# Performance work log

Measured on AMD Instinct MI355X. Metric: run time of the kernel, lower is better.

Reference implementation:

```python
import jax, jax.numpy as jnp
import numpy as np

HEADS = 16
HEAD_DIM = 64  # hidden_dim // heads = 1024 // 16


def setup_inputs() -> dict:
    key = jax.random.key(0)
    ks = jax.random.split(key, 7)
    B, S, D = 2, 2048, 1024
    x = jax.random.normal(ks[0], (B, S, D), dtype=jnp.float32)
    mask = jax.random.randint(ks[1], (B, 1, S, S), 0, 2, dtype=jnp.int32)
    scale = 1.0 / np.sqrt(D)
    Wq = jax.random.normal(ks[2], (D, D), dtype=jnp.float32) * scale
    Wk = jax.random.normal(ks[3], (D, D), dtype=jnp.float32) * scale
    Wv = jax.random.normal(ks[4], (D, D), dtype=jnp.float32) * scale
    Wo = jax.random.normal(ks[5], (D, D), dtype=jnp.float32) * scale
    bo = jnp.zeros((D,), dtype=jnp.float32)
    return {"x": x, "mask": mask, "Wq": Wq, "Wk": Wk, "Wv": Wv, "Wo": Wo, "bo": bo}


def _split_heads(t):
    # (B, S, D) -> (B, H, S, Hd)
    B, S, D = t.shape
    return t.reshape(B, S, HEADS, HEAD_DIM).transpose(0, 2, 1, 3)


def reference(x, mask, Wq, Wk, Wv, Wo, bo):
    B, S, D = x.shape
    # torch nn.Linear: y = x @ W.T (weights stored [out, in])
    q = _split_heads(x @ Wq.T)
    k = _split_heads(x @ Wk.T)
    v = _split_heads(x @ Wv.T)
    scores = jnp.einsum("bhqd,bhkd->bhqk", q, k) / jnp.sqrt(jnp.float32(HEAD_DIM))
    scores = jnp.where(mask == 1, jnp.float32(-1e9), scores)
    attn = jax.nn.softmax(scores, axis=-1)
    # dropout p=0.0 (eval) -> identity
    out = jnp.einsum("bhqk,bhkd->bhqd", attn, v)
    out = out.transpose(0, 2, 1, 3).reshape(B, S, D)
    return out @ Wo.T + bo
```

## Files before the change

kernel.cpp:

```cpp
#include <hip/hip_runtime.h>
#include <hip/hip_bf16.h>

typedef __attribute__((ext_vector_type(4))) float f32x4;
typedef __attribute__((ext_vector_type(16))) float f32x16;
typedef __attribute__((ext_vector_type(8))) short bf16x8;

#define MFMA16(a, b, c) __builtin_amdgcn_mfma_f32_16x16x32_bf16(a, b, c, 0, 0, 0)
#define MFMA32(a, b, c) __builtin_amdgcn_mfma_f32_32x32x16_bf16(a, b, c, 0, 0, 0)

#define AS1(p) ((const __attribute__((address_space(1))) void*)(p))
#define AS3(p) ((__attribute__((address_space(3))) void*)(p))

#define SWZK(r) ((((r) & 7)) ^ ((((r) >> 3) & 1) << 2))

__device__ __forceinline__ unsigned short f2bf(float f) {
  union { float f; unsigned u; } x; x.f = f;
  unsigned r = x.u + 0x7fffu + ((x.u >> 16) & 1u);
  return (unsigned short)(r >> 16);
}

__global__ __launch_bounds__(256) void convert_inputs(
    const float* __restrict__ x, const float* __restrict__ wq,
    const float* __restrict__ wk, const float* __restrict__ wv,
    const float* __restrict__ wo, const int* __restrict__ mask,
    unsigned short* __restrict__ dst, unsigned char* __restrict__ mdst) {
  const int NX = 4194304, NW = 1048576;
  if (blockIdx.x < 4096) {
    const int i = blockIdx.x * 256 + threadIdx.x;
    const long base = (long)i * 8;
    const float* src; long off; float sc = 1.0f;
    if (base < NX) { src = x; off = base; }
    else {
      long j = base - NX; int wsI = (int)(j >> 20); off = j & (NW - 1);
      src = (wsI == 0) ? wq : (wsI == 1) ? wk : (wsI == 2) ? wv : wo;
      if (wsI == 0) sc = 0.18033688f;
    }
    float4 a = *(const float4*)(src + off);
    float4 b = *(const float4*)(src + off + 4);
    uint4 o;
    o.x = (unsigned)f2bf(a.x * sc) | ((unsigned)f2bf(a.y * sc) << 16);
    o.y = (unsigned)f2bf(a.z * sc) | ((unsigned)f2bf(a.w * sc) << 16);
    o.z = (unsigned)f2bf(b.x * sc) | ((unsigned)f2bf(b.y * sc) << 16);
    o.w = (unsigned)f2bf(b.z * sc) | ((unsigned)f2bf(b.w * sc) << 16);
    ((uint4*)dst)[i] = o;
  } else {
    const int i = (blockIdx.x - 4096) * 256 + threadIdx.x;
    const int4 v = ((const int4*)mask)[i];
    uchar4 r;
    r.x = (unsigned char)v.x; r.y = (unsigned char)v.y;
    r.z = (unsigned char)v.z; r.w = (unsigned char)v.w;
    ((uchar4*)mdst)[i] = r;
  }
}

template <int BM, int BN>
__device__ __forceinline__ void gemm_nt(
    const unsigned short* __restrict__ A, const unsigned short* __restrict__ Bw,
    int m0, int n0, unsigned short* Al, unsigned short* Bl, f32x4* acc) {
  const int t = threadIdx.x;
  const int l = t & 63;
  const int w = t >> 6, wr = w >> 1, wc = w & 1;
  const int lc = l & 15, lg = l >> 4;
  constexpr int MI = BM / 32, NJ = BN / 32;
  constexpr int ASZ = BM * 32, BSZ = BN * 32;

  auto stage = [&](int buf, int kt) {
    const int k0 = kt * 32;
#pragma unroll
    for (int c = 0; c < BM / 64; ++c) {
      const int e = (t + c * 256) * 8;
      __builtin_amdgcn_global_load_lds(
          AS1(A + (size_t)(m0 + (e >> 5)) * 1024 + k0 + (e & 31)),
          AS3(Al + buf * ASZ + e), 16, 0, 0);
    }
#pragma unroll
    for (int c = 0; c < BN / 64; ++c) {
      const int e = (t + c * 256) * 8;
      __builtin_amdgcn_global_load_lds(
          AS1(Bw + (size_t)(n0 + (e >> 5)) * 1024 + k0 + (e & 31)),
          AS3(Bl + buf * BSZ + e), 16, 0, 0);
    }
  };

  stage(0, 0);
#pragma unroll 2
  for (int kt = 0; kt < 32; ++kt) {
    __syncthreads();
    if (kt + 1 < 32) stage((kt + 1) & 1, kt + 1);
    const unsigned short* Ab = Al + (kt & 1) * ASZ;
    const unsigned short* Bb = Bl + (kt & 1) * BSZ;
    bf16x8 af[MI], bfr[NJ];
#pragma unroll
    for (int i = 0; i < MI; ++i)
      af[i] = *(const bf16x8*)(Ab + (wr * (BM / 2) + i * 16 + lc) * 32 + lg * 8);
#pragma unroll
    for (int j = 0; j < NJ; ++j)
      bfr[j] = *(const bf16x8*)(Bb + (wc * (BN / 2) + j * 16 + lc) * 32 + lg * 8);
#pragma unroll
    for (int i = 0; i < MI; ++i)
#pragma unroll
      for (int j = 0; j < NJ; ++j)
        acc[i * NJ + j] = MFMA16(af[i], bfr[j], acc[i * NJ + j]);
  }
}

__global__ __launch_bounds__(256) void gemm_qkv(
    const unsigned short* __restrict__ xb,
    const unsigned short* __restrict__ wqb, const unsigned short* __restrict__ wkb,
    const unsigned short* __restrict__ wvb,
    unsigned short* __restrict__ q, unsigned short* __restrict__ k,
    unsigned short* __restrict__ vt) {
  __shared__ unsigned short Al[2 * 4096], Bl[2 * 4096];
  const int z = blockIdx.z;
  const unsigned short* Bw = (z == 0) ? wqb : (z == 1) ? wkb : wvb;
  const int m0 = blockIdx.x * 128, n0 = blockIdx.y * 128;
  f32x4 acc[16] = {};
  gemm_nt<128, 128>(xb, Bw, m0, n0, Al, Bl, acc);

  const int l = threadIdx.x & 63, w = threadIdx.x >> 6;
  const int wr = w >> 1, wc = w & 1, lc = l & 15, lg = l >> 4;

  if (z == 2) {
#pragma unroll
    for (int i = 0; i < 4; ++i)
#pragma unroll
      for (int j = 0; j < 4; ++j) {
        const int m = m0 + wr * 64 + i * 16 + lg * 4;
        const int n = n0 + wc * 64 + j * 16 + lc;
        const int b = m >> 11, s = m & 2047, hh = n >> 6, hd = n & 63;
        ushort4 pk;
        pk.x = f2bf(acc[i * 4 + j][0]); pk.y = f2bf(acc[i * 4 + j][1]);
        pk.z = f2bf(acc[i * 4 + j][2]); pk.w = f2bf(acc[i * 4 + j][3]);
        *(ushort4*)(vt + (size_t)((b << 4) + hh) * 131072 + (size_t)hd * 2048 + s) = pk;
      }
  } else {
    unsigned short* C = (z == 0) ? q : k;
#pragma unroll
    for (int i = 0; i < 4; ++i)
#pragma unroll
      for (int j = 0; j < 4; ++j)
#pragma unroll
        for (int r = 0; r < 4; ++r) {
          const int m = m0 + wr * 64 + i * 16 + lg * 4 + r;
          const int n = n0 + wc * 64 + j * 16 + lc;
          const int b = m >> 11, s = m & 2047, hh = n >> 6, hd = n & 63;
          C[(size_t)((b << 4) + hh) * 131072 + s * 64 + hd] = f2bf(acc[i * 4 + j][r]);
        }
  }
}

__global__ __launch_bounds__(256) void gemm_out(
    const unsigned short* __restrict__ ao, const unsigned short* __restrict__ wob,
    const float* __restrict__ bias, float* __restrict__ out) {
  __shared__ unsigned short Al[2 * 2048], Bl[2 * 4096];
  const int m0 = blockIdx.x * 64, n0 = blockIdx.y * 128;
  f32x4 acc[8] = {};
  gemm_nt<64, 128>(ao, wob, m0, n0, Al, Bl, acc);

  const int l = threadIdx.x & 63, w = threadIdx.x >> 6;
  const int wr = w >> 1, wc = w & 1, lc = l & 15, lg = l >> 4;
#pragma unroll
  for (int i = 0; i < 2; ++i)
#pragma unroll
    for (int j = 0; j < 4; ++j)
#pragma unroll
      for (int r = 0; r < 4; ++r) {
        const int m = m0 + wr * 32 + i * 16 + lg * 4 + r;
        const int n = n0 + wc * 64 + j * 16 + lc;
        out[(size_t)m * 1024 + n] = acc[i * 4 + j][r] + bias[n];
      }
}

__global__ __launch_bounds__(256, 2) void attn_fwd(
    const unsigned short* __restrict__ q, const unsigned short* __restrict__ k,
    const unsigned short* __restrict__ vt, const unsigned char* __restrict__ mb8,
    unsigned short* __restrict__ ao) {
  __shared__ unsigned short Kl[2][4096];
  __shared__ unsigned short Vl[2][4096];
  __shared__ unsigned char Ml[2][8192];
  __shared__ float Ll[128];
  const int orig = blockIdx.x;
  const int nid = (orig & 7) * 64 + (orig >> 3);
  const int bh = nid >> 4, b = bh >> 4, h = bh & 15;
  const int q0 = (nid & 15) * 128;
  const int t = threadIdx.x, l = t & 63, w = t >> 6;
  const int lq = l & 31, hh = l >> 5;
  const int qq = w * 32 + lq;

  const unsigned short* qp = q + ((size_t)bh * 2048 + q0 + qq) * 64;
  bf16x8 qa[4];
#pragma unroll
  for (int s = 0; s < 4; ++s) qa[s] = *(const bf16x8*)(qp + s * 16 + hh * 8);

  const unsigned short* kp = k + (size_t)bh * 131072;
  const unsigned short* vp = vt + (size_t)bh * 131072;
  const unsigned char* mp = mb8 + (size_t)b * 4194304;

  f32x16 oa[2] = {};
  float lsum = 0.f;

  auto stage = [&](int buf, int kv0) {
#pragma unroll
    for (int c = 0; c < 2; ++c) {
      const int idx = c * 256 + w * 64 + l;
      {
        const int row = idx >> 3, ch = idx & 7;
        __builtin_amdgcn_global_load_lds(
            AS1(kp + (size_t)(kv0 + row) * 64 + (ch ^ SWZK(row)) * 8),
            AS3(&Kl[buf][(c * 256 + w * 64) * 8]), 16, 0, 0);
      }
      {
        const int row = idx >> 3, ch = idx & 7;
        __builtin_amdgcn_global_load_lds(
            AS1(vp + (size_t)row * 2048 + kv0 + (ch ^ SWZK(row)) * 8),
            AS3(&Vl[buf][(c * 256 + w * 64) * 8]), 16, 0, 0);
      }
      {
        const int row = idx >> 2, ch = idx & 3;
        __builtin_amdgcn_global_load_lds(
            AS1(mp + (size_t)(q0 + row) * 2048 + kv0 + (ch ^ ((row >> 1) & 3)) * 16),
            AS3(&Ml[buf][(c * 256 + w * 64) * 16]), 16, 0, 0);
      }
    }
  };

  stage(0, 0);
  for (int tt = 0; tt < 32; ++tt) {
    const int kv0 = tt * 64;
    __syncthreads();
    if (tt + 1 < 32) stage((tt + 1) & 1, kv0 + 64);
    const unsigned short* Kb = Kl[tt & 1];
    const unsigned short* Vb = Vl[tt & 1];
    const unsigned char* Mb = Ml[tt & 1];

    f32x16 sa[2] = {};
#pragma unroll
    for (int s = 0; s < 4; ++s) {
#pragma unroll
      for (int cb = 0; cb < 2; ++cb) {
        const int row = cb * 32 + lq;
        bf16x8 kf = *(const bf16x8*)(Kb + row * 64 + (((2 * s + hh) ^ SWZK(row))) * 8);
        sa[cb] = MFMA32(kf, qa[s], sa[cb]);
      }
    }

#pragma unroll
    for (int cb = 0; cb < 2; ++cb)
#pragma unroll
      for (int g = 0; g < 4; ++g) {
        const int sdw = 8 * cb + 2 * g + hh;
        const int sl = sdw ^ (((qq >> 1) & 3) << 2);
        const unsigned mdw = *(const unsigned*)(Mb + qq * 64 + sl * 4);
#pragma unroll
        for (int i = 0; i < 4; ++i) {
          const float mf = (float)((mdw >> (8 * i)) & 255u);
          const float e = __builtin_amdgcn_exp2f(fmaf(mf, -100.f, sa[cb][4 * g + i]));
          sa[cb][4 * g + i] = e;
          lsum += e;
        }
      }

#pragma unroll
    for (int s = 0; s < 4; ++s) {
      const int cb = s >> 1, gb = 2 * (s & 1);
      unsigned pk00, pk01, pk10, pk11;
      asm("v_cvt_pk_bf16_f32 %0, %1, %2" : "=v"(pk00) : "v"(sa[cb][4 * gb + 0]), "v"(sa[cb][4 * gb + 1]));
      asm("v_cvt_pk_bf16_f32 %0, %1, %2" : "=v"(pk01) : "v"(sa[cb][4 * gb + 2]), "v"(sa[cb][4 * gb + 3]));
      asm("v_cvt_pk_bf16_f32 %0, %1, %2" : "=v"(pk10) : "v"(sa[cb][4 * gb + 4]), "v"(sa[cb][4 * gb + 5]));
      asm("v_cvt_pk_bf16_f32 %0, %1, %2" : "=v"(pk11) : "v"(sa[cb][4 * gb + 6]), "v"(sa[cb][4 * gb + 7]));
      asm("v_permlane32_swap_b32 %0, %1" : "+v"(pk00), "+v"(pk10));
      asm("v_permlane32_swap_b32 %0, %1" : "+v"(pk01), "+v"(pk11));
      union { int4 i; bf16x8 v; } fr;
      fr.i = make_int4(pk00, pk01, pk10, pk11);
#pragma unroll
      for (int db = 0; db < 2; ++db) {
        const int row = db * 32 + lq;
        bf16x8 vf = *(const bf16x8*)(Vb + row * 64 + (((2 * s + hh) ^ SWZK(row))) * 8);
        oa[db] = MFMA32(fr.v, vf, oa[db]);
      }
    }
  }

  lsum += __shfl_xor(lsum, 32, 64);
  Ll[qq] = __builtin_amdgcn_rcpf(lsum);
  __syncthreads();

#pragma unroll
  for (int r = 0; r < 16; ++r) {
    const int row = (r & 3) + 8 * (r >> 2) + 4 * hh;
    const float inv = Ll[w * 32 + row];
    unsigned short* dst = ao + ((size_t)b * 2048 + q0 + w * 32 + row) * 1024 + h * 64;
    dst[lq] = f2bf(oa[0][r] * inv);
    dst[32 + lq] = f2bf(oa[1][r] * inv);
  }
}

extern "C" void kernel_launch(void* const* d_in, const int* in_sizes, int n_in,
                              void* d_out, int out_size, void* d_ws, size_t ws_size,
                              hipStream_t stream) {
  const float* x = (const float*)d_in[0];
  const int* mask = (const int*)d_in[1];
  const float* Wq = (const float*)d_in[2];
  const float* Wk = (const float*)d_in[3];
  const float* Wv = (const float*)d_in[4];
  const float* Wo = (const float*)d_in[5];
  const float* bo = (const float*)d_in[6];

  unsigned short* ws = (unsigned short*)d_ws;
  unsigned short* xb = ws;
  unsigned short* wqb = xb + 4194304;
  unsigned short* wkb = wqb + 1048576;
  unsigned short* wvb = wkb + 1048576;
  unsigned short* wob = wvb + 1048576;
  unsigned short* qb = wob + 1048576;
  unsigned short* kb = qb + 4194304;
  unsigned short* vtb = kb + 4194304;
  unsigned short* aob = vtb + 4194304;
  unsigned char* mb8 = (unsigned char*)(aob + 4194304);

  convert_inputs<<<dim3(12288), dim3(256), 0, stream>>>(x, Wq, Wk, Wv, Wo, mask, ws, mb8);
  gemm_qkv<<<dim3(32, 8, 3), dim3(256), 0, stream>>>(xb, wqb, wkb, wvb, qb, kb, vtb);
  attn_fwd<<<dim3(512), dim3(256), 0, stream>>>(qb, kb, vtb, mb8, aob);
  gemm_out<<<dim3(64, 8), dim3(256), 0, stream>>>(aob, wob, bo, (float*)d_out);
}
```

Measured before the change: 228.8 us.

## Split attention over KV halves, shrink GEMM tiles, load mask directly to registers

```diff
diff --git a/kernel.cpp b/kernel.cpp
--- a/kernel.cpp
+++ b/kernel.cpp
@@ -17,6 +17,12 @@
   union { float f; unsigned u; } x; x.f = f;
   unsigned r = x.u + 0x7fffu + ((x.u >> 16) & 1u);
   return (unsigned short)(r >> 16);
+}
+__device__ __forceinline__ float bfl(unsigned u) {
+  union { unsigned u; float f; } x; x.u = u << 16; return x.f;
+}
+__device__ __forceinline__ float bfh(unsigned u) {
+  union { unsigned u; float f; } x; x.u = u & 0xffff0000u; return x.f;
 }
 
 __global__ __launch_bounds__(256) void convert_inputs(
@@ -104,18 +110,18 @@
   }
 }
 
-__global__ __launch_bounds__(256) void gemm_qkv(
+__global__ __launch_bounds__(256, 5) void gemm_qkv(
     const unsigned short* __restrict__ xb,
     const unsigned short* __restrict__ wqb, const unsigned short* __restrict__ wkb,
     const unsigned short* __restrict__ wvb,
     unsigned short* __restrict__ q, unsigned short* __restrict__ k,
     unsigned short* __restrict__ vt) {
-  __shared__ unsigned short Al[2 * 4096], Bl[2 * 4096];
+  __shared__ unsigned short Al[2 * 4096], Bl[2 * 2048];
   const int z = blockIdx.z;
   const unsigned short* Bw = (z == 0) ? wqb : (z == 1) ? wkb : wvb;
-  const int m0 = blockIdx.x * 128, n0 = blockIdx.y * 128;
-  f32x4 acc[16] = {};
-  gemm_nt<128, 128>(xb, Bw, m0, n0, Al, Bl, acc);
+  const int m0 = blockIdx.x * 128, n0 = blockIdx.y * 64;
+  f32x4 acc[8] = {};
+  gemm_nt<128, 64>(xb, Bw, m0, n0, Al, Bl, acc);
 
   const int l = threadIdx.x & 63, w = threadIdx.x >> 6;
   const int wr = w >> 1, wc = w & 1, lc = l & 15, lg = l >> 4;
@@ -124,13 +130,13 @@
 #pragma unroll
     for (int i = 0; i < 4; ++i)
 #pragma unroll
-      for (int j = 0; j < 4; ++j) {
+      for (int j = 0; j < 2; ++j) {
         const int m = m0 + wr * 64 + i * 16 + lg * 4;
-        const int n = n0 + wc * 64 + j * 16 + lc;
+        const int n = n0 + wc * 32 + j * 16 + lc;
         const int b = m >> 11, s = m & 2047, hh = n >> 6, hd = n & 63;
         ushort4 pk;
-        pk.x = f2bf(acc[i * 4 + j][0]); pk.y = f2bf(acc[i * 4 + j][1]);
-        pk.z = f2bf(acc[i * 4 + j][2]); pk.w = f2bf(acc[i * 4 + j][3]);
+        pk.x = f2bf(acc[i * 2 + j][0]); pk.y = f2bf(acc[i * 2 + j][1]);
+        pk.z = f2bf(acc[i * 2 + j][2]); pk.w = f2bf(acc[i * 2 + j][3]);
         *(ushort4*)(vt + (size_t)((b << 4) + hh) * 131072 + (size_t)hd * 2048 + s) = pk;
       }
   } else {
@@ -138,49 +144,49 @@
 #pragma unroll
     for (int i = 0; i < 4; ++i)
 #pragma unroll
-      for (int j = 0; j < 4; ++j)
+      for (int j = 0; j < 2; ++j)
 #pragma unroll
         for (int r = 0; r < 4; ++r) {
           const int m = m0 + wr * 64 + i * 16 + lg * 4 + r;
-          const int n = n0 + wc * 64 + j * 16 + lc;
+          const int n = n0 + wc * 32 + j * 16 + lc;
           const int b = m >> 11, s = m & 2047, hh = n >> 6, hd = n & 63;
-          C[(size_t)((b << 4) + hh) * 131072 + s * 64 + hd] = f2bf(acc[i * 4 + j][r]);
+          C[(size_t)((b << 4) + hh) * 131072 + s * 64 + hd] = f2bf(acc[i * 2 + j][r]);
         }
   }
 }
 
-__global__ __launch_bounds__(256) void gemm_out(
+__global__ __launch_bounds__(256, 4) void gemm_out(
     const unsigned short* __restrict__ ao, const unsigned short* __restrict__ wob,
     const float* __restrict__ bias, float* __restrict__ out) {
-  __shared__ unsigned short Al[2 * 2048], Bl[2 * 4096];
-  const int m0 = blockIdx.x * 64, n0 = blockIdx.y * 128;
-  f32x4 acc[8] = {};
-  gemm_nt<64, 128>(ao, wob, m0, n0, Al, Bl, acc);
+  __shared__ unsigned short Al[2 * 2048], Bl[2 * 2048];
+  const int m0 = blockIdx.x * 64, n0 = blockIdx.y * 64;
+  f32x4 acc[4] = {};
+  gemm_nt<64, 64>(ao, wob, m0, n0, Al, Bl, acc);
 
   const int l = threadIdx.x & 63, w = threadIdx.x >> 6;
   const int wr = w >> 1, wc = w & 1, lc = l & 15, lg = l >> 4;
 #pragma unroll
   for (int i = 0; i < 2; ++i)
 #pragma unroll
-    for (int j = 0; j < 4; ++j)
+    for (int j = 0; j < 2; ++j)
 #pragma unroll
       for (int r = 0; r < 4; ++r) {
         const int m = m0 + wr * 32 + i * 16 + lg * 4 + r;
-        const int n = n0 + wc * 64 + j * 16 + lc;
-        out[(size_t)m * 1024 + n] = acc[i * 4 + j][r] + bias[n];
-      }
-}
-
-__global__ __launch_bounds__(256, 2) void attn_fwd(
+        const int n = n0 + wc * 32 + j * 16 + lc;
+        out[(size_t)m * 1024 + n] = acc[i * 2 + j][r] + bias[n];
+      }
+}
+
+__global__ __launch_bounds__(256, 4) void attn_fwd(
     const unsigned short* __restrict__ q, const unsigned short* __restrict__ k,
     const unsigned short* __restrict__ vt, const unsigned char* __restrict__ mb8,
-    unsigned short* __restrict__ ao) {
+    unsigned short* __restrict__ p0, unsigned short* __restrict__ p1,
+    float* __restrict__ lpart) {
   __shared__ unsigned short Kl[2][4096];
   __shared__ unsigned short Vl[2][4096];
-  __shared__ unsigned char Ml[2][8192];
-  __shared__ float Ll[128];
   const int orig = blockIdx.x;
   const int nid = (orig & 7) * 64 + (orig >> 3);
+  const int half = blockIdx.y;
   const int bh = nid >> 4, b = bh >> 4, h = bh & 15;
   const int q0 = (nid & 15) * 128;
   const int t = threadIdx.x, l = t & 63, w = t >> 6;
@@ -194,7 +200,7 @@
 
   const unsigned short* kp = k + (size_t)bh * 131072;
   const unsigned short* vp = vt + (size_t)bh * 131072;
-  const unsigned char* mp = mb8 + (size_t)b * 4194304;
+  const unsigned char* mrow = mb8 + (size_t)b * 4194304 + (size_t)(q0 + qq) * 2048;
 
   f32x16 oa[2] = {};
   float lsum = 0.f;
@@ -203,37 +209,35 @@
 #pragma unroll
     for (int c = 0; c < 2; ++c) {
       const int idx = c * 256 + w * 64 + l;
-      {
-        const int row = idx >> 3, ch = idx & 7;
-        __builtin_amdgcn_global_load_lds(
-            AS1(kp + (size_t)(kv0 + row) * 64 + (ch ^ SWZK(row)) * 8),
-            AS3(&Kl[buf][(c * 256 + w * 64) * 8]), 16, 0, 0);
-      }
-      {
-        const int row = idx >> 3, ch = idx & 7;
-        __builtin_amdgcn_global_load_lds(
-            AS1(vp + (size_t)row * 2048 + kv0 + (ch ^ SWZK(row)) * 8),
-            AS3(&Vl[buf][(c * 256 + w * 64) * 8]), 16, 0, 0);
-      }
-      {
-        const int row = idx >> 2, ch = idx & 3;
-        __builtin_amdgcn_global_load_lds(
-            AS1(mp + (size_t)(q0 + row) * 2048 + kv0 + (ch ^ ((row >> 1) & 3)) * 16),
-            AS3(&Ml[buf][(c * 256 + w * 64) * 16]), 16, 0, 0);
-      }
+      const int row = idx >> 3, ch = idx & 7;
+      __builtin_amdgcn_global_load_lds(
+          AS1(kp + (size_t)(kv0 + row) * 64 + (ch ^ SWZK(row)) * 8),
+          AS3(&Kl[buf][(c * 256 + w * 64) * 8]), 16, 0, 0);
+      __builtin_amdgcn_global_load_lds(
+          AS1(vp + (size_t)row * 2048 + kv0 + (ch ^ SWZK(row)) * 8),
+          AS3(&Vl[buf][(c * 256 + w * 64) * 8]), 16, 0, 0);
     }
   };
 
-  stage(0, 0);
-  for (int tt = 0; tt < 32; ++tt) {
-    const int kv0 = tt * 64;
+  const int kvbase = half * 1024;
+  stage(0, kvbase);
+  for (int tt = 0; tt < 16; ++tt) {
+    const int kv0 = kvbase + tt * 64;
     __syncthreads();
-    if (tt + 1 < 32) stage((tt + 1) & 1, kv0 + 64);
+
+    unsigned mreg[8];
+#pragma unroll
+    for (int cb = 0; cb < 2; ++cb)
+#pragma unroll
+      for (int g = 0; g < 4; ++g)
+        mreg[cb * 4 + g] = *(const unsigned*)(mrow + kv0 + cb * 32 + g * 8 + hh * 4);
+
+    if (tt + 1 < 16) stage((tt + 1) & 1, kv0 + 64);
     const unsigned short* Kb = Kl[tt & 1];
     const unsigned short* Vb = Vl[tt & 1];
-    const unsigned char* Mb = Ml[tt & 1];
 
     f32x16 sa[2] = {};
+    __builtin_amdgcn_s_setprio(1);
 #pragma unroll
     for (int s = 0; s < 4; ++s) {
 #pragma unroll
@@ -243,14 +247,13 @@
         sa[cb] = MFMA32(kf, qa[s], sa[cb]);
       }
     }
+    __builtin_amdgcn_s_setprio(0);
 
 #pragma unroll
     for (int cb = 0; cb < 2; ++cb)
 #pragma unroll
       for (int g = 0; g < 4; ++g) {
-        const int sdw = 8 * cb + 2 * g + hh;
-        const int sl = sdw ^ (((qq >> 1) & 3) << 2);
-        const unsigned mdw = *(const unsigned*)(Mb + qq * 64 + sl * 4);
+        const unsigned mdw = mreg[cb * 4 + g];
 #pragma unroll
         for (int i = 0; i < 4; ++i) {
           const float mf = (float)((mdw >> (8 * i)) & 255u);
@@ -260,6 +263,7 @@
         }
       }
 
+    __builtin_amdgcn_s_setprio(1);
 #pragma unroll
     for (int s = 0; s < 4; ++s) {
       const int cb = s >> 1, gb = 2 * (s & 1);
@@ -279,20 +283,38 @@
         oa[db] = MFMA32(fr.v, vf, oa[db]);
       }
     }
-  }
-
-  lsum += __shfl_xor(lsum, 32, 64);
-  Ll[qq] = __builtin_amdgcn_rcpf(lsum);
-  __syncthreads();
-
+    __builtin_amdgcn_s_setprio(0);
+  }
+
+  unsigned short* op = half ? p1 : p0;
 #pragma unroll
   for (int r = 0; r < 16; ++r) {
     const int row = (r & 3) + 8 * (r >> 2) + 4 * hh;
-    const float inv = Ll[w * 32 + row];
-    unsigned short* dst = ao + ((size_t)b * 2048 + q0 + w * 32 + row) * 1024 + h * 64;
-    dst[lq] = f2bf(oa[0][r] * inv);
-    dst[32 + lq] = f2bf(oa[1][r] * inv);
-  }
+    unsigned short* dst = op + ((size_t)b * 2048 + q0 + w * 32 + row) * 1024 + h * 64;
+    dst[lq] = f2bf(oa[0][r]);
+    dst[32 + lq] = f2bf(oa[1][r]);
+  }
+  lsum += __shfl_xor(lsum, 32, 64);
+  if (hh == 0) lpart[half * 65536 + bh * 2048 + q0 + qq] = lsum;
+}
+
+__global__ __launch_bounds__(256) void combine_o(
+    const unsigned short* __restrict__ p1, const float* __restrict__ lp,
+    unsigned short* __restrict__ ao) {
+  const int i = blockIdx.x * 256 + threadIdx.x;
+  const long base = (long)i * 8;
+  const int bi = (int)(base >> 21), s = (int)((base >> 10) & 2047),
+            h = (int)((base >> 6) & 15);
+  const int lidx = ((bi << 4) + h) * 2048 + s;
+  const float inv = __builtin_amdgcn_rcpf(lp[lidx] + lp[65536 + lidx]);
+  uint4 a = ((const uint4*)ao)[i];
+  uint4 bq = ((const uint4*)p1)[i];
+  uint4 o;
+  o.x = (unsigned)f2bf((bfl(a.x) + bfl(bq.x)) * inv) | ((unsigned)f2bf((bfh(a.x) + bfh(bq.x)) * inv) << 16);
+  o.y = (unsigned)f2bf((bfl(a.y) + bfl(bq.y)) * inv) | ((unsigned)f2bf((bfh(a.y) + bfh(bq.y)) * inv) << 16);
+  o.z = (unsigned)f2bf((bfl(a.z) + bfl(bq.z)) * inv) | ((unsigned)f2bf((bfh(a.z) + bfh(bq.z)) * inv) << 16);
+  o.w = (unsigned)f2bf((bfl(a.w) + bfl(bq.w)) * inv) | ((unsigned)f2bf((bfh(a.w) + bfh(bq.w)) * inv) << 16);
+  ((uint4*)ao)[i] = o;
 }
 
 extern "C" void kernel_launch(void* const* d_in, const int* in_sizes, int n_in,
@@ -317,9 +339,11 @@
   unsigned short* vtb = kb + 4194304;
   unsigned short* aob = vtb + 4194304;
   unsigned char* mb8 = (unsigned char*)(aob + 4194304);
+  float* lpart = (float*)wqb;
 
   convert_inputs<<<dim3(12288), dim3(256), 0, stream>>>(x, Wq, Wk, Wv, Wo, mask, ws, mb8);
-  gemm_qkv<<<dim3(32, 8, 3), dim3(256), 0, stream>>>(xb, wqb, wkb, wvb, qb, kb, vtb);
-  attn_fwd<<<dim3(512), dim3(256), 0, stream>>>(qb, kb, vtb, mb8, aob);
-  gemm_out<<<dim3(64, 8), dim3(256), 0, stream>>>(aob, wob, bo, (float*)d_out);
-}
+  gemm_qkv<<<dim3(32, 16, 3), dim3(256), 0, stream>>>(xb, wqb, wkb, wvb, qb, kb, vtb);
+  attn_fwd<<<dim3(512, 2), dim3(256), 0, stream>>>(qb, kb, vtb, mb8, aob, xb, lpart);
+  combine_o<<<dim3(2048), dim3(256), 0, stream>>>(xb, lpart, aob);
+  gemm_out<<<dim3(64, 16), dim3(256), 0, stream>>>(aob, wob, bo, (float*)d_out);
+}
```

Result: slower. 256.3 us (+12.0%).
